# Kernel tuning notes

Measured on AMD Instinct MI355X. Metric: run time of the kernel, lower is better.

Reference implementation:

```python
import jax, jax.numpy as jnp
import numpy as np

SIGMA = 1.0
NUM_CLASSES = 10


def setup_inputs() -> dict:
    key = jax.random.key(0)
    k1, k2, k3, k4 = jax.random.split(key, 4)
    ns, nt, d = 4096, 4096, 256
    return {
        "source_feature": jax.random.normal(k1, (ns, d), dtype=jnp.float32),
        "source_label": jax.random.randint(k2, (ns,), 0, NUM_CLASSES),
        "target_feature": jax.random.normal(k3, (nt, d), dtype=jnp.float32),
        "class_weight": jax.random.uniform(k4, (NUM_CLASSES,), dtype=jnp.float32),
    }


def _rbf_gram(x, y, sigma):
    # K[i, j] = exp(-||x_i - y_j||^2 / (2*sigma)); [n, m]
    x2 = jnp.sum(x * x, axis=-1)  # [n]
    y2 = jnp.sum(y * y, axis=-1)  # [m]
    sq = x2[:, None] + y2[None, :] - 2.0 * (x @ y.T)
    sq = jnp.maximum(sq, 0.0)
    return jnp.exp(-sq / (2.0 * sigma))


def reference(source_feature, source_label, target_feature, class_weight):
    ns = source_feature.shape[0]
    nt = target_feature.shape[0]
    w = class_weight[source_label]          # [ns] per-sample weight
    n = jnp.sum(w)                          # weighted source count

    Kss = _rbf_gram(source_feature, source_feature, SIGMA)  # [ns, ns]
    Ktt = _rbf_gram(target_feature, target_feature, SIGMA)  # [nt, nt]
    Kst = _rbf_gram(source_feature, target_feature, SIGMA)  # [ns, nt]

    first = jnp.einsum('i,ij,j->', w, Kss, w)
    sec = jnp.sum(Ktt)
    third = jnp.einsum('i,ij->', w, Kst)

    return first / (n * n) + sec / (nt * nt) - 2.0 * third / (n * nt)
```

## Files before the change

kernel.cpp:

```cpp
#include <hip/hip_runtime.h>
#include <hip/hip_bf16.h>


typedef float f32x4 __attribute__((ext_vector_type(4)));
typedef unsigned int u32x4 __attribute__((ext_vector_type(4)));

#define D 256

static __device__ __forceinline__ unsigned int f32_to_e4m3(float f) {
    unsigned int u = __float_as_uint(f);
    unsigned int sg = (u >> 24) & 0x80;
    unsigned int um = u & 0x7FFFFFFF;
    unsigned int r = um + 0x0007FFFF + ((um >> 20) & 1);
    int e8 = (int)((r >> 23) & 0xFF) - 127 + 7;
    unsigned int m8 = (r >> 20) & 7;
    if (e8 <= 0) return sg;
    if (e8 > 15 || (e8 == 15 && m8 == 7)) return sg | 0x7E;
    return sg | ((unsigned)e8 << 3) | m8;
}


__global__ __launch_bounds__(256) void prep_kernel(
    const float* __restrict__ sf, const float* __restrict__ tf,
    const int* __restrict__ lbl, const float* __restrict__ cw,
    unsigned char* __restrict__ sfb, unsigned char* __restrict__ tfb,
    float* __restrict__ x2s, float* __restrict__ x2t,
    float* __restrict__ wv, int ns)
{
    __shared__ unsigned int ldsb[1024];

    int gb = blockIdx.x;
    int nsg = ns >> 4;
    bool is_src = gb < nsg;
    int gloc = is_src ? gb : gb - nsg;
    const float* src = (is_src ? sf : tf) + (size_t)gloc * 16 * D;
    unsigned char* dstb = (is_src ? sfb : tfb) + (size_t)gloc * 4096;

    int tid = threadIdx.x;
    int l = tid & 63;
    int w = tid >> 6;

    if (is_src && tid < 16) {
        int r = gloc * 16 + tid;
        wv[r] = cw[lbl[r]];
    }

    #pragma unroll
    for (int p = 0; p < 4; ++p) {
        int row = 4 * p + w;
        int k0 = l * 4;
        float4 v = *(const float4*)(src + row * D + k0);
        unsigned int packed = f32_to_e4m3(v.x)
                            | (f32_to_e4m3(v.y) << 8)
                            | (f32_to_e4m3(v.z) << 16)
                            | (f32_to_e4m3(v.w) << 24);
        int s  = l >> 3;
        int kg = (l >> 1) & 3;
        int off = s * 512 + (row + 16 * kg) * 8 + (l & 1) * 4;
        ldsb[off >> 2] = packed;

        float ps = v.x * v.x + v.y * v.y + v.z * v.z + v.w * v.w;
        #pragma unroll
        for (int o = 32; o; o >>= 1) ps += __shfl_xor(ps, o);
        if (l == 0) {
            int gr = gloc * 16 + row;
            if (is_src) x2s[gr] = ps; else x2t[gr] = ps;
        }
    }
    __syncthreads();
    u32x4 val = ((const u32x4*)ldsb)[tid];
    __builtin_nontemporal_store(val, ((u32x4*)dstb) + tid);
}

__global__ __launch_bounds__(512, 4) void gram_kernel(
    const unsigned char* __restrict__ sfb, const unsigned char* __restrict__ tfb,
    const float* __restrict__ x2s, const float* __restrict__ x2t,
    const float* __restrict__ wv, float* __restrict__ bout,
    int ti_s, int ti_t)
{
    int tri_s = ti_s * (ti_s + 1) / 2;
    int tri_t = ti_t * (ti_t + 1) / 2;
    int blk = blockIdx.x;

    int mode, bi, bj;
    const unsigned char *X, *Y;
    const float *x2xp, *x2yp;
    if (blk < tri_s + tri_t) {
        int T, idx;
        if (blk < tri_s) { mode = 0; idx = blk; T = ti_s; X = sfb; Y = sfb; x2xp = x2s; x2yp = x2s; }
        else { mode = 1; idx = blk - tri_s; T = ti_t; X = tfb; Y = tfb; x2xp = x2t; x2yp = x2t; }
        bi = (int)((2.0f * T + 1.0f -
                    sqrtf((float)((2 * T + 1) * (2 * T + 1) - 8 * idx))) * 0.5f);
        if (bi < 0) bi = 0;
        if (bi > T - 1) bi = T - 1;
        int base = bi * (2 * T - bi + 1) / 2;
        while (base > idx) { --bi; base = bi * (2 * T - bi + 1) / 2; }
        while (idx >= base + (T - bi)) { base += (T - bi); ++bi; }
        bj = bi + (idx - base);
    } else {
        int idx = blk - tri_s - tri_t;
        mode = 2; bi = idx / ti_t; bj = idx % ti_t;
        X = sfb; Y = tfb; x2xp = x2s; x2yp = x2t;
    }
    float factor = (mode != 2 && bi != bj) ? 2.0f : 1.0f;

    int wid = threadIdx.x >> 6;
    int lane = threadIdx.x & 63;
    int wr = wid >> 2, wc = wid & 3;
    int R0 = bi * 128 + wr * 64;
    int C0 = bj * 128 + wc * 32;

    const unsigned char* XA = X + (size_t)(bi * 8 + wr * 4) * 4096 + lane * 8;
    const unsigned char* YB = Y + (size_t)(bj * 8 + wc * 2) * 4096 + lane * 8;

    f32x4 acc[4][2] = {};
    long af[2][4], bf_[2][2];
    #pragma unroll
    for (int m = 0; m < 4; ++m) af[0][m] = *(const long*)(XA + m * 4096);
    #pragma unroll
    for (int n = 0; n < 2; ++n) bf_[0][n] = *(const long*)(YB + n * 4096);

    #pragma unroll
    for (int s = 0; s < 8; ++s) {
        const int cur = s & 1;
        if (s < 7) {
            #pragma unroll
            for (int m = 0; m < 4; ++m)
                af[cur ^ 1][m] = *(const long*)(XA + m * 4096 + (s + 1) * 512);
            #pragma unroll
            for (int n = 0; n < 2; ++n)
                bf_[cur ^ 1][n] = *(const long*)(YB + n * 4096 + (s + 1) * 512);
        }
        #pragma unroll
        for (int m = 0; m < 4; ++m)
            #pragma unroll
            for (int n = 0; n < 2; ++n)
                acc[m][n] = __builtin_amdgcn_mfma_f32_16x16x32_fp8_fp8(
                    af[cur][m], bf_[cur][n], acc[m][n], 0, 0, 0);
    }

    int crow = (lane >> 4) * 4;
    int ccol = lane & 15;
    float x2yc[2];
    #pragma unroll
    for (int n = 0; n < 2; ++n) x2yc[n] = x2yp[C0 + 16 * n + ccol];

    float s = 0.0f;
    #pragma unroll
    for (int m = 0; m < 4; ++m) {
        #pragma unroll
        for (int r = 0; r < 4; ++r) {
            int gr = R0 + 16 * m + crow + r;
            float rx2 = x2xp[gr];
            float sq0 = fmaxf(rx2 + x2yc[0] - 2.0f * acc[m][0][r], 0.0f);
            float sq1 = fmaxf(rx2 + x2yc[1] - 2.0f * acc[m][1][r], 0.0f);
            float mn = fminf(sq0, sq1);
            if (__any(mn < 180.0f)) {
                float rw = (mode != 1) ? wv[gr] : 1.0f;
                float sqv[2] = {sq0, sq1};
                #pragma unroll
                for (int n = 0; n < 2; ++n) {
                    int gc = C0 + 16 * n + ccol;
                    float K = __expf(-0.5f * sqv[n]);
                    if (mode != 2 && gr == gc) K = 0.0f;
                    float wf = (mode == 0) ? rw * wv[gc] : rw;
                    s += wf * K;
                }
            }
        }
    }
    s *= factor;
    #pragma unroll
    for (int o = 32; o; o >>= 1) s += __shfl_xor(s, o);

    __shared__ float bsum[8];
    if (lane == 0) bsum[wid] = s;
    __syncthreads();
    if (threadIdx.x == 0) {
        float t0 = 0.0f;
        #pragma unroll
        for (int i = 0; i < 8; ++i) t0 += bsum[i];
        bout[blk] = t0;
    }
}

__global__ __launch_bounds__(1024) void reduce_kernel(
    const float* __restrict__ wv, int ns,
    const float* __restrict__ bout, int tri_s, int tri_t, int nb,
    float* __restrict__ out, int nt)
{
    int tid = threadIdx.x;
    float n = 0.0f, dsq = 0.0f, a0 = 0.0f, a1 = 0.0f, a2 = 0.0f;
    for (int i = tid; i < ns; i += 1024) {
        float w = wv[i];
        n += w;
        dsq += w * w;
    }
    for (int i = tid; i < nb; i += 1024) {
        float v = bout[i];
        if (i < tri_s) a0 += v;
        else if (i < tri_s + tri_t) a1 += v;
        else a2 += v;
    }
    #pragma unroll
    for (int o = 32; o; o >>= 1) {
        n   += __shfl_xor(n, o);
        dsq += __shfl_xor(dsq, o);
        a0  += __shfl_xor(a0, o);
        a1  += __shfl_xor(a1, o);
        a2  += __shfl_xor(a2, o);
    }
    __shared__ float ln[16], ld[16], l0[16], l1[16], l2[16];
    int w = tid >> 6;
    if ((tid & 63) == 0) { ln[w] = n; ld[w] = dsq; l0[w] = a0; l1[w] = a1; l2[w] = a2; }
    __syncthreads();
    if (tid == 0) {
        float N = 0, DQ = 0, A0 = 0, A1 = 0, A2 = 0;
        #pragma unroll
        for (int i = 0; i < 16; ++i) {
            N += ln[i]; DQ += ld[i]; A0 += l0[i]; A1 += l1[i]; A2 += l2[i];
        }
        float fnt = (float)nt;
        out[0] = (A0 + DQ) / (N * N) + (A1 + fnt) / (fnt * fnt)
               - 2.0f * A2 / (N * fnt);
    }
}

extern "C" void kernel_launch(void* const* d_in, const int* in_sizes, int n_in,
                              void* d_out, int out_size, void* d_ws, size_t ws_size,
                              hipStream_t stream) {
    const float* sf = (const float*)d_in[0];
    const int* lbl = (const int*)d_in[1];
    const float* tf = (const float*)d_in[2];
    const float* cw = (const float*)d_in[3];
    float* out = (float*)d_out;

    int ns = in_sizes[1];
    int d = in_sizes[0] / ns;
    int nt = in_sizes[2] / d;

    char* p = (char*)d_ws;
    unsigned char* sfb = (unsigned char*)p;  p += (size_t)ns * d;
    unsigned char* tfb = (unsigned char*)p;  p += (size_t)nt * d;
    float* x2s = (float*)p;                  p += (size_t)ns * sizeof(float);
    float* x2t = (float*)p;                  p += (size_t)nt * sizeof(float);
    float* wv  = (float*)p;                  p += (size_t)ns * sizeof(float);
    float* bout = (float*)p;

    prep_kernel<<<(ns + nt) / 16, 256, 0, stream>>>(sf, tf, lbl, cw, sfb, tfb,
                                                    x2s, x2t, wv, ns);

    int ti_s = ns / 128, ti_t = nt / 128;
    int tri_s = ti_s * (ti_s + 1) / 2;
    int tri_t = ti_t * (ti_t + 1) / 2;
    int nblocks = tri_s + tri_t + ti_s * ti_t;
    gram_kernel<<<nblocks, 512, 0, stream>>>(sfb, tfb, x2s, x2t, wv, bout,
                                             ti_s, ti_t);

    reduce_kernel<<<1, 1024, 0, stream>>>(wv, ns, bout, tri_s, tri_t, nblocks,
                                          out, nt);
}
```

Measured before the change: 51.54 us.

## Fuse final reduction into gram kernel via last-block counter, enlarge per-wave tiles

Result: slower. 83.19 us (+61.4%).

```diff
diff --git a/kernel.cpp b/kernel.cpp
--- a/kernel.cpp
+++ b/kernel.cpp
@@ -25,7 +25,7 @@
     const int* __restrict__ lbl, const float* __restrict__ cw,
     unsigned char* __restrict__ sfb, unsigned char* __restrict__ tfb,
     float* __restrict__ x2s, float* __restrict__ x2t,
-    float* __restrict__ wv, int ns)
+    float* __restrict__ wv, int* __restrict__ counter, int ns)
 {
     __shared__ unsigned int ldsb[1024];
 
@@ -40,6 +40,10 @@
     int l = tid & 63;
     int w = tid >> 6;
 
+    if (gb == 0 && tid == 0)
+        __hip_atomic_store(counter, 0, __ATOMIC_RELAXED,
+                           __HIP_MEMORY_SCOPE_AGENT);
+
     if (is_src && tid < 16) {
         int r = gloc * 16 + tid;
         wv[r] = cw[lbl[r]];
@@ -48,8 +52,7 @@
     #pragma unroll
     for (int p = 0; p < 4; ++p) {
         int row = 4 * p + w;
-        int k0 = l * 4;
-        float4 v = *(const float4*)(src + row * D + k0);
+        float4 v = *(const float4*)(src + row * D + l * 4);
         unsigned int packed = f32_to_e4m3(v.x)
                             | (f32_to_e4m3(v.y) << 8)
                             | (f32_to_e4m3(v.z) << 16)
@@ -72,14 +75,16 @@
     __builtin_nontemporal_store(val, ((u32x4*)dstb) + tid);
 }
 
-__global__ __launch_bounds__(512, 4) void gram_kernel(
+__global__ __launch_bounds__(256, 3) void gram_kernel(
     const unsigned char* __restrict__ sfb, const unsigned char* __restrict__ tfb,
     const float* __restrict__ x2s, const float* __restrict__ x2t,
     const float* __restrict__ wv, float* __restrict__ bout,
+    int* __restrict__ counter, float* __restrict__ out,
     int ti_s, int ti_t)
 {
     int tri_s = ti_s * (ti_s + 1) / 2;
     int tri_t = ti_t * (ti_t + 1) / 2;
+    int NT = tri_s + tri_t + ti_s * ti_t;
     int blk = blockIdx.x;
 
     int mode, bi, bj;
@@ -106,44 +111,47 @@
 
     int wid = threadIdx.x >> 6;
     int lane = threadIdx.x & 63;
-    int wr = wid >> 2, wc = wid & 3;
+    int wr = wid >> 1, wc = wid & 1;
     int R0 = bi * 128 + wr * 64;
-    int C0 = bj * 128 + wc * 32;
-
-    const unsigned char* XA = X + (size_t)(bi * 8 + wr * 4) * 4096 + lane * 8;
-    const unsigned char* YB = Y + (size_t)(bj * 8 + wc * 2) * 4096 + lane * 8;
-
-    f32x4 acc[4][2] = {};
-    long af[2][4], bf_[2][2];
-    #pragma unroll
-    for (int m = 0; m < 4; ++m) af[0][m] = *(const long*)(XA + m * 4096);
-    #pragma unroll
-    for (int n = 0; n < 2; ++n) bf_[0][n] = *(const long*)(YB + n * 4096);
-
+    int C0 = bj * 128 + wc * 64;
+
+    const unsigned char* XA = X + (size_t)(R0 >> 4) * 4096 + lane * 8;
+    const unsigned char* YB = Y + (size_t)(C0 >> 4) * 4096 + lane * 8;
+
+    f32x4 acc[4][4] = {};
+    long af[4][4], bf_[4][4];
+    #pragma unroll
+    for (int sp = 0; sp < 3; ++sp) {
+        #pragma unroll
+        for (int m = 0; m < 4; ++m) {
+            af[sp][m]  = *(const long*)(XA + (size_t)(m * 8 + sp) * 512);
+            bf_[sp][m] = *(const long*)(YB + (size_t)(m * 8 + sp) * 512);
+        }
+    }
     #pragma unroll
     for (int s = 0; s < 8; ++s) {
-        const int cur = s & 1;
-        if (s < 7) {
+        const int cur = s & 3;
+        if (s < 5) {
+            const int pf = (s + 3) & 3;
             #pragma unroll
-            for (int m = 0; m < 4; ++m)
-                af[cur ^ 1][m] = *(const long*)(XA + m * 4096 + (s + 1) * 512);
-            #pragma unroll
-            for (int n = 0; n < 2; ++n)
-                bf_[cur ^ 1][n] = *(const long*)(YB + n * 4096 + (s + 1) * 512);
+            for (int m = 0; m < 4; ++m) {
+                af[pf][m]  = *(const long*)(XA + (size_t)(m * 8 + s + 3) * 512);
+                bf_[pf][m] = *(const long*)(YB + (size_t)(m * 8 + s + 3) * 512);
+            }
         }
         #pragma unroll
         for (int m = 0; m < 4; ++m)
             #pragma unroll
-            for (int n = 0; n < 2; ++n)
+            for (int n = 0; n < 4; ++n)
                 acc[m][n] = __builtin_amdgcn_mfma_f32_16x16x32_fp8_fp8(
                     af[cur][m], bf_[cur][n], acc[m][n], 0, 0, 0);
     }
 
     int crow = (lane >> 4) * 4;
     int ccol = lane & 15;
-    float x2yc[2];
-    #pragma unroll
-    for (int n = 0; n < 2; ++n) x2yc[n] = x2yp[C0 + 16 * n + ccol];
+    float x2yc[4];
+    #pragma unroll
+    for (int n = 0; n < 4; ++n) x2yc[n] = x2yp[C0 + 16 * n + ccol];
 
     float s = 0.0f;
     #pragma unroll
@@ -154,12 +162,14 @@
             float rx2 = x2xp[gr];
             float sq0 = fmaxf(rx2 + x2yc[0] - 2.0f * acc[m][0][r], 0.0f);
             float sq1 = fmaxf(rx2 + x2yc[1] - 2.0f * acc[m][1][r], 0.0f);
-            float mn = fminf(sq0, sq1);
+            float sq2 = fmaxf(rx2 + x2yc[2] - 2.0f * acc[m][2][r], 0.0f);
+            float sq3 = fmaxf(rx2 + x2yc[3] - 2.0f * acc[m][3][r], 0.0f);
+            float mn = fminf(fminf(sq0, sq1), fminf(sq2, sq3));
             if (__any(mn < 180.0f)) {
                 float rw = (mode != 1) ? wv[gr] : 1.0f;
-                float sqv[2] = {sq0, sq1};
+                float sqv[4] = {sq0, sq1, sq2, sq3};
                 #pragma unroll
-                for (int n = 0; n < 2; ++n) {
+                for (int n = 0; n < 4; ++n) {
                     int gc = C0 + 16 * n + ccol;
                     float K = __expf(-0.5f * sqv[n]);
                     if (mode != 2 && gr == gc) K = 0.0f;
@@ -173,31 +183,30 @@
     #pragma unroll
     for (int o = 32; o; o >>= 1) s += __shfl_xor(s, o);
 
-    __shared__ float bsum[8];
+    __shared__ float bsum[4];
+    __shared__ int tks;
     if (lane == 0) bsum[wid] = s;
     __syncthreads();
     if (threadIdx.x == 0) {
-        float t0 = 0.0f;
-        #pragma unroll
-        for (int i = 0; i < 8; ++i) t0 += bsum[i];
-        bout[blk] = t0;
-    }
-}
-
-__global__ __launch_bounds__(1024) void reduce_kernel(
-    const float* __restrict__ wv, int ns,
-    const float* __restrict__ bout, int tri_s, int tri_t, int nb,
-    float* __restrict__ out, int nt)
-{
+        float v = (bsum[0] + bsum[1]) + (bsum[2] + bsum[3]);
+        __hip_atomic_store(&bout[blk], v, __ATOMIC_RELEASE,
+                           __HIP_MEMORY_SCOPE_AGENT);
+        tks = __hip_atomic_fetch_add(counter, 1, __ATOMIC_ACQ_REL,
+                                     __HIP_MEMORY_SCOPE_AGENT);
+    }
+    __syncthreads();
+    if (tks != NT - 1) return;
+
     int tid = threadIdx.x;
+    int ns = ti_s * 128, ntr = ti_t * 128;
     float n = 0.0f, dsq = 0.0f, a0 = 0.0f, a1 = 0.0f, a2 = 0.0f;
-    for (int i = tid; i < ns; i += 1024) {
+    for (int i = tid; i < ns; i += 256) {
         float w = wv[i];
-        n += w;
-        dsq += w * w;
-    }
-    for (int i = tid; i < nb; i += 1024) {
-        float v = bout[i];
+        n += w; dsq += w * w;
+    }
+    for (int i = tid; i < NT; i += 256) {
+        float v = __hip_atomic_load(&bout[i], __ATOMIC_ACQUIRE,
+                                    __HIP_MEMORY_SCOPE_AGENT);
         if (i < tri_s) a0 += v;
         else if (i < tri_s + tri_t) a1 += v;
         else a2 += v;
@@ -210,17 +219,16 @@
         a1  += __shfl_xor(a1, o);
         a2  += __shfl_xor(a2, o);
     }
-    __shared__ float ln[16], ld[16], l0[16], l1[16], l2[16];
-    int w = tid >> 6;
-    if ((tid & 63) == 0) { ln[w] = n; ld[w] = dsq; l0[w] = a0; l1[w] = a1; l2[w] = a2; }
+    __shared__ float ln[4], ld[4], l0[4], l1[4], l2[4];
+    if (lane == 0) { ln[wid] = n; ld[wid] = dsq; l0[wid] = a0; l1[wid] = a1; l2[wid] = a2; }
     __syncthreads();
     if (tid == 0) {
         float N = 0, DQ = 0, A0 = 0, A1 = 0, A2 = 0;
         #pragma unroll
-        for (int i = 0; i < 16; ++i) {
+        for (int i = 0; i < 4; ++i) {
             N += ln[i]; DQ += ld[i]; A0 += l0[i]; A1 += l1[i]; A2 += l2[i];
         }
-        float fnt = (float)nt;
+        float fnt = (float)ntr;
         out[0] = (A0 + DQ) / (N * N) + (A1 + fnt) / (fnt * fnt)
                - 2.0f * A2 / (N * fnt);
     }
@@ -245,18 +253,16 @@
     float* x2s = (float*)p;                  p += (size_t)ns * sizeof(float);
     float* x2t = (float*)p;                  p += (size_t)nt * sizeof(float);
     float* wv  = (float*)p;                  p += (size_t)ns * sizeof(float);
-    float* bout = (float*)p;
-
-    prep_kernel<<<(ns + nt) / 16, 256, 0, stream>>>(sf, tf, lbl, cw, sfb, tfb,
-                                                    x2s, x2t, wv, ns);
-
     int ti_s = ns / 128, ti_t = nt / 128;
     int tri_s = ti_s * (ti_s + 1) / 2;
     int tri_t = ti_t * (ti_t + 1) / 2;
-    int nblocks = tri_s + tri_t + ti_s * ti_t;
-    gram_kernel<<<nblocks, 512, 0, stream>>>(sfb, tfb, x2s, x2t, wv, bout,
-                                             ti_s, ti_t);
-
-    reduce_kernel<<<1, 1024, 0, stream>>>(wv, ns, bout, tri_s, tri_t, nblocks,
-                                          out, nt);
-}
+    int NT = tri_s + tri_t + ti_s * ti_t;
+    float* bout = (float*)p;                 p += (size_t)NT * sizeof(float);
+    int* counter = (int*)p;
+
+    prep_kernel<<<(ns + nt) / 16, 256, 0, stream>>>(sf, tf, lbl, cw, sfb, tfb,
+                                                    x2s, x2t, wv, counter, ns);
+
+    gram_kernel<<<NT, 256, 0, stream>>>(sfb, tfb, x2s, x2t, wv, bout,
+                                        counter, out, ti_s, ti_t);
+}
```
